# Optimization experiments

Measured on AMD Instinct MI355X. Metric: run time of the kernel, lower is better.

## Reference

```python
import jax, jax.numpy as jnp
import numpy as np

B, T, C, NH = 8, 1024, 768, 12

def setup_inputs() -> dict:
    key = jax.random.key(0)
    k1, k2, k3 = jax.random.split(key, 3)
    x = jax.random.normal(k1, (B, T, C), dtype=jnp.float32)
    Wqkv = jax.random.normal(k2, (C, 3 * C), dtype=jnp.float32) * 0.02
    bqkv = jnp.zeros((3 * C,), dtype=jnp.float32)
    Wproj = jax.random.normal(k3, (C, C), dtype=jnp.float32) * 0.02
    bproj = jnp.zeros((C,), dtype=jnp.float32)
    return {"x": x, "Wqkv": Wqkv, "bqkv": bqkv, "Wproj": Wproj, "bproj": bproj}

def reference(x, Wqkv, bqkv, Wproj, bproj):
    b, t, c = x.shape
    hs = c // NH
    qkv = x @ Wqkv + bqkv  # [B,T,3C]
    q, k, v = jnp.split(qkv, 3, axis=2)
    # [B,T,C] -> [B,NH,T,hs]
    q = q.reshape(b, t, NH, hs).transpose(0, 2, 1, 3)
    k = k.reshape(b, t, NH, hs).transpose(0, 2, 1, 3)
    v = v.reshape(b, t, NH, hs).transpose(0, 2, 1, 3)
    att = jnp.einsum('bhqd,bhkd->bhqk', q, k) * (hs ** -0.5)
    causal = jnp.tril(jnp.ones((t, t), dtype=bool))
    att = jnp.where(causal[None, None], att, jnp.finfo(att.dtype).min)
    att = jax.nn.softmax(att, axis=-1)
    y = jnp.einsum('bhqk,bhkd->bhqd', att, v)
    y = y.transpose(0, 2, 1, 3).reshape(b, t, c)
    return y @ Wproj + bproj
```

## Files before the change

### kernel.cpp

```cpp
#include <hip/hip_runtime.h>

constexpr int Bb  = 8;
constexpr int Tt  = 1024;
constexpr int Cc  = 768;
constexpr int NHh = 12;
constexpr int HS  = 64;
constexpr int C3  = 3 * Cc;

typedef short bf16x8 __attribute__((ext_vector_type(8)));
typedef float f32x4  __attribute__((ext_vector_type(4)));

__device__ inline short bf16r(float f) {
    unsigned u = __float_as_uint(f);
    u += 0x7FFF + ((u >> 16) & 1);
    return (short)(u >> 16);
}
__device__ inline short bf16h(float f) {
    return (short)((__float_as_uint(f) + 0x8000u) >> 16);
}

__global__ __launch_bounds__(256)
void prep_all(const float* __restrict__ x, const float* __restrict__ Wqkv,
              const float* __restrict__ Wproj, short* __restrict__ xb,
              short* __restrict__ wqkvT, short* __restrict__ wprojT) {
    int bid = blockIdx.x;
    constexpr int XBLK = (Bb * Tt * Cc) / 1024;
    constexpr int QT   = (C3 / 32) * (Cc / 32);
    if (bid < XBLK) {
        const int i = (bid * 256 + threadIdx.x) * 4;
        float4 v = *(const float4*)(x + i);
        short4 o;
        o.x = bf16r(v.x); o.y = bf16r(v.y); o.z = bf16r(v.z); o.w = bf16r(v.w);
        *(short4*)(xb + i) = o;
        return;
    }
    bid -= XBLK;
    const float* src; short* dst; int C;
    if (bid < QT) { src = Wqkv;  dst = wqkvT;  C = C3; }
    else          { bid -= QT; src = Wproj; dst = wprojT; C = Cc; }
    const int tcx = bid % (C / 32), tcy = bid / (C / 32);
    __shared__ short tile[32][33];
    const int tx = threadIdx.x & 31, ty = threadIdx.x >> 5;
#pragma unroll
    for (int rr = 0; rr < 4; ++rr) {
        const int r = ty * 4 + rr;
        tile[r][tx] = bf16r(src[(size_t)(tcy * 32 + r) * C + tcx * 32 + tx]);
    }
    __syncthreads();
#pragma unroll
    for (int rr = 0; rr < 4; ++rr) {
        const int orow = ty * 4 + rr;
        dst[(size_t)(tcx * 32 + orow) * Cc + tcy * 32 + tx] = tile[tx][orow];
    }
}

__global__ __launch_bounds__(256)
void transpose_v(const short* __restrict__ qkv, short* __restrict__ vt) {
    __shared__ short tile[64][65];
    const int bh = blockIdx.y;
    const int b = bh / NHh, h = bh % NHh;
    const int t0 = blockIdx.x * 64;
    const int tx = threadIdx.x & 63, ty = threadIdx.x >> 6;
    const short* src = qkv + ((size_t)b * Tt + t0) * C3 + 2 * Cc + h * HS;
#pragma unroll
    for (int r = 0; r < 16; ++r)
        tile[ty * 16 + r][tx] = src[(size_t)(ty * 16 + r) * C3 + tx];
    __syncthreads();
    short* dst = vt + (size_t)bh * HS * Tt + t0;
#pragma unroll
    for (int r = 0; r < 16; ++r)
        dst[(size_t)(ty * 16 + r) * Tt + tx] = tile[tx][ty * 16 + r];
}

template <int MI, int OB>
__global__ __launch_bounds__(256)
void gemm_mfma_bias(const short* __restrict__ A, const short* __restrict__ Bt,
                    const float* __restrict__ bias, void* __restrict__ Cout,
                    int M, int N, int K) {
    constexpr int TM = MI * 32;
    __shared__ __align__(16) short Als[2][TM * 32];
    __shared__ __align__(16) short Bls[2][128 * 32];

    const int t = threadIdx.x, w = t >> 6, lane = t & 63;

    const int flat = blockIdx.y * gridDim.x + blockIdx.x;
    const int mPer = gridDim.y >> 3;
    const int idx  = flat >> 3;
    const int my   = (flat & 7) * mPer + idx % mPer;
    const int nx   = idx / mPer;
    const int m0 = my * TM, n0 = nx * 128;

    const int sr = t >> 2;
    const int lg = ((t & 3) ^ ((t >> 3) & 3)) * 8;

    const short* Ag[MI / 2];
#pragma unroll
    for (int q = 0; q < MI / 2; ++q)
        Ag[q] = A + (size_t)(m0 + q * 64 + sr) * K + lg;
    const short* Bg[2];
#pragma unroll
    for (int q = 0; q < 2; ++q)
        Bg[q] = Bt + (size_t)(n0 + q * 64 + sr) * K + lg;

    const int wq = w * 1024;

    const int wm = (w >> 1) * (MI * 16), wn = (w & 1) * 64;
    const int laneM = lane & 15, laneG = lane >> 4;
    const int kx = (laneG ^ ((laneM >> 1) & 3)) * 8;

    f32x4 acc[MI][4] = {};

    const int nk = K / 32;

#pragma unroll
    for (int q = 0; q < MI / 2; ++q)
        __builtin_amdgcn_global_load_lds(
            (const __attribute__((address_space(1))) void*)(Ag[q]),
            (__attribute__((address_space(3))) void*)((char*)&Als[0][0] + q * 4096 + wq), 16, 0, 0);
#pragma unroll
    for (int q = 0; q < 2; ++q)
        __builtin_amdgcn_global_load_lds(
            (const __attribute__((address_space(1))) void*)(Bg[q]),
            (__attribute__((address_space(3))) void*)((char*)&Bls[0][0] + q * 4096 + wq), 16, 0, 0);

    for (int kt = 0; kt < nk; ++kt) {
        __syncthreads();

        const short* Ab = &Als[kt & 1][0];
        const short* Bb = &Bls[kt & 1][0];
        bf16x8 af[MI], bfr[4];
#pragma unroll
        for (int i = 0; i < MI; ++i)
            af[i] = *(const bf16x8*)&Ab[(wm + i * 16 + laneM) * 32 + kx];
#pragma unroll
        for (int j = 0; j < 4; ++j)
            bfr[j] = *(const bf16x8*)&Bb[(wn + j * 16 + laneM) * 32 + kx];

        if (kt + 1 < nk) {
            const int b = (kt + 1) & 1, ko = (kt + 1) * 32;
#pragma unroll
            for (int q = 0; q < MI / 2; ++q)
                __builtin_amdgcn_global_load_lds(
                    (const __attribute__((address_space(1))) void*)(Ag[q] + ko),
                    (__attribute__((address_space(3))) void*)((char*)&Als[b][0] + q * 4096 + wq), 16, 0, 0);
#pragma unroll
            for (int q = 0; q < 2; ++q)
                __builtin_amdgcn_global_load_lds(
                    (const __attribute__((address_space(1))) void*)(Bg[q] + ko),
                    (__attribute__((address_space(3))) void*)((char*)&Bls[b][0] + q * 4096 + wq), 16, 0, 0);
        }

#pragma unroll
        for (int i = 0; i < MI; ++i)
#pragma unroll
            for (int j = 0; j < 4; ++j)
                acc[i][j] = __builtin_amdgcn_mfma_f32_16x16x32_bf16(
                    af[i], bfr[j], acc[i][j], 0, 0, 0);
    }

    const int rowBase = m0 + wm + laneG * 4;
    const int colBase = n0 + wn + laneM;
#pragma unroll
    for (int j = 0; j < 4; ++j) {
        const int col = colBase + j * 16;
        const float bv = bias[col];
#pragma unroll
        for (int i = 0; i < MI; ++i) {
#pragma unroll
            for (int r = 0; r < 4; ++r) {
                const int row = rowBase + i * 16 + r;
                const float v = acc[i][j][r] + bv;
                if (OB) ((short*)Cout)[(size_t)row * N + col] = bf16r(v);
                else    ((float*)Cout)[(size_t)row * N + col] = v;
            }
        }
    }
}

__global__ __launch_bounds__(256)
void flash_attn(const short* __restrict__ qkv, const short* __restrict__ vt,
                short* __restrict__ y) {
    const int bh = blockIdx.x % (Bb * NHh);
    const int pi = blockIdx.x / (Bb * NHh);
    const int h  = bh % NHh, b = bh / NHh;
    const int t = threadIdx.x, w = t >> 6, lane = t & 63;
    const int laneM = lane & 15, laneG = lane >> 4;

    __shared__ short Kls[2][64 * 64];
    __shared__ short Vls[2][64 * 64];
    __shared__ short Pls[4][16 * 72];

    const size_t bT = (size_t)b * Tt;

    bf16x8 onesb;
#pragma unroll
    for (int j = 0; j < 8; ++j) onesb[j] = (short)0x3F80;

    const int srow = t >> 3;
    const int gpos = t & 7;
    const int gs0 = (gpos ^ (srow & 7)) * 8;

    const short* Kbase = qkv + (bT + srow) * C3 + Cc + h * HS + gs0;
    const short* Vbase = vt + ((size_t)bh * HS + srow) * Tt + gs0;

    auto stage = [&](int kt, int buf) {
        const short* Kg = Kbase + (size_t)kt * 64 * C3;
        const short* Vg = Vbase + kt * 64;
        char* KB = (char*)&Kls[buf][0] + w * 1024;
        char* VB = (char*)&Vls[buf][0] + w * 1024;
        __builtin_amdgcn_global_load_lds(
            (const __attribute__((address_space(1))) void*)Kg,
            (__attribute__((address_space(3))) void*)(KB), 16, 0, 0);
        __builtin_amdgcn_global_load_lds(
            (const __attribute__((address_space(1))) void*)(Kg + 32 * C3),
            (__attribute__((address_space(3))) void*)(KB + 4096), 16, 0, 0);
        __builtin_amdgcn_global_load_lds(
            (const __attribute__((address_space(1))) void*)Vg,
            (__attribute__((address_space(3))) void*)(VB), 16, 0, 0);
        __builtin_amdgcn_global_load_lds(
            (const __attribute__((address_space(1))) void*)(Vg + 32 * Tt),
            (__attribute__((address_space(3))) void*)(VB + 4096), 16, 0, 0);
    };

    constexpr float cexp = 0.18033688f;
    constexpr float moff = -5.7707801f;

#pragma unroll 1
    for (int sub = 0; sub < 2; ++sub) {
        const int qt = sub ? (15 - pi) : pi;
        const int q0 = qt * 64;

        const short* qp = qkv + (bT + q0 + w * 16 + laneM) * C3 + h * HS;
        const bf16x8 qf0 = *(const bf16x8*)(qp + laneG * 8);
        const bf16x8 qf1 = *(const bf16x8*)(qp + 32 + laneG * 8);

        f32x4 oacc[4] = {};
        f32x4 lacc   = {};

        __syncthreads();
        stage(0, 0);

#pragma unroll 1
        for (int kt = 0; kt <= qt; ++kt) {
            __syncthreads();
            if (kt < qt) stage(kt + 1, (kt + 1) & 1);

            const short* Kb = &Kls[kt & 1][0];
            const short* Vb = &Vls[kt & 1][0];

            f32x4 sacc[4] = {};
            __builtin_amdgcn_s_setprio(1);
#pragma unroll
            for (int ks = 0; ks < 2; ++ks) {
                const bf16x8 qf = ks ? qf1 : qf0;
#pragma unroll
                for (int nb = 0; nb < 4; ++nb) {
                    const int key = nb * 16 + laneM;
                    const bf16x8 kf = *(const bf16x8*)
                        &Kb[key * 64 + (((ks << 2) + laneG) ^ (key & 7)) * 8];
                    sacc[nb] = __builtin_amdgcn_mfma_f32_16x16x32_bf16(
                        qf, kf, sacc[nb], 0, 0, 0);
                }
            }
            __builtin_amdgcn_s_setprio(0);

            if (kt == qt) {
#pragma unroll
                for (int nb = 0; nb < 4; ++nb) {
                    const int col = nb * 16 + laneM;
#pragma unroll
                    for (int r = 0; r < 4; ++r) {
                        const int row = w * 16 + laneG * 4 + r;
                        if (col > row) sacc[nb][r] = -1e30f;
                    }
                }
            }

            short* Pw = &Pls[w][0];
#pragma unroll
            for (int r = 0; r < 4; ++r)
#pragma unroll
                for (int nb = 0; nb < 4; ++nb) {
                    const float pv = exp2f(fmaf(sacc[nb][r], cexp, moff));
                    Pw[(laneG * 4 + r) * 72 + nb * 16 + laneM] = bf16h(pv);
                }

            __builtin_amdgcn_s_setprio(1);
#pragma unroll
            for (int ks = 0; ks < 2; ++ks) {
                const bf16x8 pf = *(const bf16x8*)&Pw[laneM * 72 + ks * 32 + laneG * 8];
                lacc = __builtin_amdgcn_mfma_f32_16x16x32_bf16(pf, onesb, lacc, 0, 0, 0);
#pragma unroll
                for (int nb = 0; nb < 4; ++nb) {
                    const int d = nb * 16 + laneM;
                    const bf16x8 vf = *(const bf16x8*)
                        &Vb[d * 64 + (((ks << 2) + laneG) ^ (d & 7)) * 8];
                    oacc[nb] = __builtin_amdgcn_mfma_f32_16x16x32_bf16(
                        pf, vf, oacc[nb], 0, 0, 0);
                }
            }
            __builtin_amdgcn_s_setprio(0);
        }

        short* yp = y + (bT + q0 + w * 16) * Cc + h * HS;
#pragma unroll
        for (int r = 0; r < 4; ++r) {
            const float inv = 1.f / lacc[r];
#pragma unroll
            for (int nb = 0; nb < 4; ++nb)
                yp[(size_t)(laneG * 4 + r) * Cc + nb * 16 + laneM] = bf16r(oacc[nb][r] * inv);
        }
    }
}

extern "C" void kernel_launch(void* const* d_in, const int* in_sizes, int n_in,
                              void* d_out, int out_size, void* d_ws, size_t ws_size,
                              hipStream_t stream) {
    const float* x     = (const float*)d_in[0];
    const float* Wqkv  = (const float*)d_in[1];
    const float* bqkv  = (const float*)d_in[2];
    const float* Wproj = (const float*)d_in[3];
    const float* bproj = (const float*)d_in[4];

    constexpr int M = Bb * Tt;
    short* xb     = (short*)d_ws;
    short* wqkvT  = xb     + (size_t)M * Cc;
    short* wprojT = wqkvT  + (size_t)C3 * Cc;
    short* qkv    = wprojT + (size_t)Cc * Cc;
    short* yatt   = qkv    + (size_t)M * C3;
    short* vt     = yatt   + (size_t)M * Cc;

    constexpr int PREP_BLOCKS = (M * Cc) / 1024 + (C3 / 32) * (Cc / 32) + (Cc / 32) * (Cc / 32);
    prep_all<<<dim3(PREP_BLOCKS), dim3(256), 0, stream>>>(x, Wqkv, Wproj, xb, wqkvT, wprojT);

    gemm_mfma_bias<4, 1><<<dim3(C3 / 128, M / 128), dim3(256), 0, stream>>>(
        xb, wqkvT, bqkv, qkv, M, C3, Cc);

    transpose_v<<<dim3(Tt / 64, Bb * NHh), dim3(256), 0, stream>>>(qkv, vt);

    flash_attn<<<dim3(Bb * NHh * 8), dim3(256), 0, stream>>>(qkv, vt, yatt);

    gemm_mfma_bias<2, 0><<<dim3(Cc / 128, M / 64), dim3(256), 0, stream>>>(
        yatt, wprojT, bproj, (float*)d_out, M, Cc, Cc);
}
```

Baseline: 182.7 us.

## Pass softmax probabilities via cross-lane permutes instead of LDS round-trip

The QK^T MFMA operands are swapped so each lane holds scores transposed (keys along rows), letting probabilities be packed to bf16 with v_cvt_pk_bf16_f32 and redistributed into the PV A-operand layout via ds_bpermute rather than being written to and re-read from a per-wave LDS buffer. The causal mask indexing is adjusted for the transposed layout, the P shared buffer is removed, and launch bounds request 5 waves/blocks per SIMD. This removes LDS stores/loads and the associated waits per tile, at the cost of 16 bpermutes plus selects per tile and possible register pressure from the occupancy hint.

```diff
diff --git a/kernel.cpp b/kernel.cpp
--- a/kernel.cpp
+++ b/kernel.cpp
@@ -9,14 +9,12 @@
 
 typedef short bf16x8 __attribute__((ext_vector_type(8)));
 typedef float f32x4  __attribute__((ext_vector_type(4)));
+typedef int   i32x4  __attribute__((ext_vector_type(4)));
 
 __device__ inline short bf16r(float f) {
     unsigned u = __float_as_uint(f);
     u += 0x7FFF + ((u >> 16) & 1);
     return (short)(u >> 16);
-}
-__device__ inline short bf16h(float f) {
-    return (short)((__float_as_uint(f) + 0x8000u) >> 16);
 }
 
 __global__ __launch_bounds__(256)
@@ -177,7 +175,7 @@
     }
 }
 
-__global__ __launch_bounds__(256)
+__global__ __launch_bounds__(256, 5)
 void flash_attn(const short* __restrict__ qkv, const short* __restrict__ vt,
                 short* __restrict__ y) {
     const int bh = blockIdx.x % (Bb * NHh);
@@ -188,7 +186,6 @@
 
     __shared__ short Kls[2][64 * 64];
     __shared__ short Vls[2][64 * 64];
-    __shared__ short Pls[4][16 * 72];
 
     const size_t bT = (size_t)b * Tt;
 
@@ -202,6 +199,10 @@
 
     const short* Kbase = qkv + (bT + srow) * C3 + Cc + h * HS + gs0;
     const short* Vbase = vt + ((size_t)bh * HS + srow) * Tt + gs0;
+
+    const int addrLo = (laneM + ((laneG & 1) << 5)) << 2;
+    const int addrHi = addrLo + 64;
+    const bool hi32 = (lane >= 32);
 
     auto stage = [&](int kt, int buf) {
         const short* Kg = Kbase + (size_t)kt * 64 * C3;
@@ -259,7 +260,7 @@
                     const bf16x8 kf = *(const bf16x8*)
                         &Kb[key * 64 + (((ks << 2) + laneG) ^ (key & 7)) * 8];
                     sacc[nb] = __builtin_amdgcn_mfma_f32_16x16x32_bf16(
-                        qf, kf, sacc[nb], 0, 0, 0);
+                        kf, qf, sacc[nb], 0, 0, 0);
                 }
             }
             __builtin_amdgcn_s_setprio(0);
@@ -267,36 +268,51 @@
             if (kt == qt) {
 #pragma unroll
                 for (int nb = 0; nb < 4; ++nb) {
-                    const int col = nb * 16 + laneM;
+                    const int qrow = w * 16 + laneM;
 #pragma unroll
                     for (int r = 0; r < 4; ++r) {
-                        const int row = w * 16 + laneG * 4 + r;
-                        if (col > row) sacc[nb][r] = -1e30f;
+                        const int key = nb * 16 + laneG * 4 + r;
+                        if (key > qrow) sacc[nb][r] = -1e30f;
                     }
                 }
             }
 
-            short* Pw = &Pls[w][0];
-#pragma unroll
-            for (int r = 0; r < 4; ++r)
-#pragma unroll
-                for (int nb = 0; nb < 4; ++nb) {
-                    const float pv = exp2f(fmaf(sacc[nb][r], cexp, moff));
-                    Pw[(laneG * 4 + r) * 72 + nb * 16 + laneM] = bf16h(pv);
+            unsigned pk[4][2];
+#pragma unroll
+            for (int nb = 0; nb < 4; ++nb) {
+                const float e0 = exp2f(fmaf(sacc[nb][0], cexp, moff));
+                const float e1 = exp2f(fmaf(sacc[nb][1], cexp, moff));
+                const float e2 = exp2f(fmaf(sacc[nb][2], cexp, moff));
+                const float e3 = exp2f(fmaf(sacc[nb][3], cexp, moff));
+                asm("v_cvt_pk_bf16_f32 %0, %1, %2" : "=v"(pk[nb][0]) : "v"(e0), "v"(e1));
+                asm("v_cvt_pk_bf16_f32 %0, %1, %2" : "=v"(pk[nb][1]) : "v"(e2), "v"(e3));
+            }
+
+            bf16x8 pf[2];
+#pragma unroll
+            for (int ks = 0; ks < 2; ++ks) {
+                i32x4 dw;
+#pragma unroll
+                for (int jd = 0; jd < 4; ++jd) {
+                    const int addr = (jd & 2) ? addrHi : addrLo;
+                    const int lo = __builtin_amdgcn_ds_bpermute(addr, (int)pk[2 * ks][jd & 1]);
+                    const int hi = __builtin_amdgcn_ds_bpermute(addr, (int)pk[2 * ks + 1][jd & 1]);
+                    dw[jd] = hi32 ? hi : lo;
                 }
+                pf[ks] = *(const bf16x8*)&dw;
+            }
 
             __builtin_amdgcn_s_setprio(1);
 #pragma unroll
             for (int ks = 0; ks < 2; ++ks) {
-                const bf16x8 pf = *(const bf16x8*)&Pw[laneM * 72 + ks * 32 + laneG * 8];
-                lacc = __builtin_amdgcn_mfma_f32_16x16x32_bf16(pf, onesb, lacc, 0, 0, 0);
+                lacc = __builtin_amdgcn_mfma_f32_16x16x32_bf16(pf[ks], onesb, lacc, 0, 0, 0);
 #pragma unroll
                 for (int nb = 0; nb < 4; ++nb) {
                     const int d = nb * 16 + laneM;
                     const bf16x8 vf = *(const bf16x8*)
                         &Vb[d * 64 + (((ks << 2) + laneG) ^ (d & 7)) * 8];
                     oacc[nb] = __builtin_amdgcn_mfma_f32_16x16x32_bf16(
-                        pf, vf, oacc[nb], 0, 0, 0);
+                        pf[ks], vf, oacc[nb], 0, 0, 0);
                 }
             }
             __builtin_amdgcn_s_setprio(0);
```

Result: no change. 183.8 us (+0.6%).

## Use two waves per flash-attention block with 32 query rows each

Applied to the files above, without the earlier changes.

The attention kernel drops from four waves of 16 query rows to two waves of 32 rows each. K and V fragments are read from LDS once into registers and reused across both 16-row groups, which halves LDS fragment traffic per MFMA. Each thread now issues four staging loads per tile instead of two. The cost is higher register pressure per wave, and there are half as many waves per block to hide latency, which may reduce occupancy or overlap.

```diff
diff --git a/kernel.cpp b/kernel.cpp
--- a/kernel.cpp
+++ b/kernel.cpp
@@ -177,7 +177,7 @@
     }
 }
 
-__global__ __launch_bounds__(256)
+__global__ __launch_bounds__(128)
 void flash_attn(const short* __restrict__ qkv, const short* __restrict__ vt,
                 short* __restrict__ y) {
     const int bh = blockIdx.x % (Bb * NHh);
@@ -188,7 +188,7 @@
 
     __shared__ short Kls[2][64 * 64];
     __shared__ short Vls[2][64 * 64];
-    __shared__ short Pls[4][16 * 72];
+    __shared__ short Pls[2][32 * 72];
 
     const size_t bT = (size_t)b * Tt;
 
@@ -208,18 +208,16 @@
         const short* Vg = Vbase + kt * 64;
         char* KB = (char*)&Kls[buf][0] + w * 1024;
         char* VB = (char*)&Vls[buf][0] + w * 1024;
-        __builtin_amdgcn_global_load_lds(
-            (const __attribute__((address_space(1))) void*)Kg,
-            (__attribute__((address_space(3))) void*)(KB), 16, 0, 0);
-        __builtin_amdgcn_global_load_lds(
-            (const __attribute__((address_space(1))) void*)(Kg + 32 * C3),
-            (__attribute__((address_space(3))) void*)(KB + 4096), 16, 0, 0);
-        __builtin_amdgcn_global_load_lds(
-            (const __attribute__((address_space(1))) void*)Vg,
-            (__attribute__((address_space(3))) void*)(VB), 16, 0, 0);
-        __builtin_amdgcn_global_load_lds(
-            (const __attribute__((address_space(1))) void*)(Vg + 32 * Tt),
-            (__attribute__((address_space(3))) void*)(VB + 4096), 16, 0, 0);
+#pragma unroll
+        for (int i = 0; i < 4; ++i)
+            __builtin_amdgcn_global_load_lds(
+                (const __attribute__((address_space(1))) void*)(Kg + (size_t)i * 16 * C3),
+                (__attribute__((address_space(3))) void*)(KB + i * 2048), 16, 0, 0);
+#pragma unroll
+        for (int i = 0; i < 4; ++i)
+            __builtin_amdgcn_global_load_lds(
+                (const __attribute__((address_space(1))) void*)(Vg + (size_t)i * 16 * Tt),
+                (__attribute__((address_space(3))) void*)(VB + i * 2048), 16, 0, 0);
     };
 
     constexpr float cexp = 0.18033688f;
@@ -230,12 +228,16 @@
         const int qt = sub ? (15 - pi) : pi;
         const int q0 = qt * 64;
 
-        const short* qp = qkv + (bT + q0 + w * 16 + laneM) * C3 + h * HS;
-        const bf16x8 qf0 = *(const bf16x8*)(qp + laneG * 8);
-        const bf16x8 qf1 = *(const bf16x8*)(qp + 32 + laneG * 8);
-
-        f32x4 oacc[4] = {};
-        f32x4 lacc   = {};
+        const short* qp0 = qkv + (bT + q0 + w * 32 + laneM) * C3 + h * HS;
+        const short* qp1 = qp0 + (size_t)16 * C3;
+        bf16x8 qf[2][2];
+        qf[0][0] = *(const bf16x8*)(qp0 + laneG * 8);
+        qf[0][1] = *(const bf16x8*)(qp0 + 32 + laneG * 8);
+        qf[1][0] = *(const bf16x8*)(qp1 + laneG * 8);
+        qf[1][1] = *(const bf16x8*)(qp1 + 32 + laneG * 8);
+
+        f32x4 oacc[2][4] = {};
+        f32x4 lacc[2]    = {};
 
         __syncthreads();
         stage(0, 0);
@@ -248,67 +250,91 @@
             const short* Kb = &Kls[kt & 1][0];
             const short* Vb = &Vls[kt & 1][0];
 
-            f32x4 sacc[4] = {};
-            __builtin_amdgcn_s_setprio(1);
-#pragma unroll
-            for (int ks = 0; ks < 2; ++ks) {
-                const bf16x8 qf = ks ? qf1 : qf0;
+            bf16x8 kf[2][4];
+#pragma unroll
+            for (int ks = 0; ks < 2; ++ks)
 #pragma unroll
                 for (int nb = 0; nb < 4; ++nb) {
                     const int key = nb * 16 + laneM;
-                    const bf16x8 kf = *(const bf16x8*)
+                    kf[ks][nb] = *(const bf16x8*)
                         &Kb[key * 64 + (((ks << 2) + laneG) ^ (key & 7)) * 8];
-                    sacc[nb] = __builtin_amdgcn_mfma_f32_16x16x32_bf16(
-                        qf, kf, sacc[nb], 0, 0, 0);
                 }
+
+            f32x4 sacc[2][4] = {};
+            __builtin_amdgcn_s_setprio(1);
+#pragma unroll
+            for (int mg = 0; mg < 2; ++mg)
+#pragma unroll
+                for (int ks = 0; ks < 2; ++ks)
+#pragma unroll
+                    for (int nb = 0; nb < 4; ++nb)
+                        sacc[mg][nb] = __builtin_amdgcn_mfma_f32_16x16x32_bf16(
+                            qf[mg][ks], kf[ks][nb], sacc[mg][nb], 0, 0, 0);
+            __builtin_amdgcn_s_setprio(0);
+
+            if (kt == qt) {
+#pragma unroll
+                for (int mg = 0; mg < 2; ++mg)
+#pragma unroll
+                    for (int nb = 0; nb < 4; ++nb) {
+                        const int col = nb * 16 + laneM;
+#pragma unroll
+                        for (int r = 0; r < 4; ++r) {
+                            const int row = w * 32 + mg * 16 + laneG * 4 + r;
+                            if (col > row) sacc[mg][nb][r] = -1e30f;
+                        }
+                    }
             }
-            __builtin_amdgcn_s_setprio(0);
-
-            if (kt == qt) {
-#pragma unroll
-                for (int nb = 0; nb < 4; ++nb) {
-                    const int col = nb * 16 + laneM;
-#pragma unroll
-                    for (int r = 0; r < 4; ++r) {
-                        const int row = w * 16 + laneG * 4 + r;
-                        if (col > row) sacc[nb][r] = -1e30f;
+
+            short* Pw = &Pls[w][0];
+#pragma unroll
+            for (int mg = 0; mg < 2; ++mg)
+#pragma unroll
+                for (int r = 0; r < 4; ++r)
+#pragma unroll
+                    for (int nb = 0; nb < 4; ++nb) {
+                        const float pv = exp2f(fmaf(sacc[mg][nb][r], cexp, moff));
+                        Pw[(mg * 16 + laneG * 4 + r) * 72 + nb * 16 + laneM] = bf16h(pv);
                     }
-                }
-            }
-
-            short* Pw = &Pls[w][0];
-#pragma unroll
-            for (int r = 0; r < 4; ++r)
-#pragma unroll
-                for (int nb = 0; nb < 4; ++nb) {
-                    const float pv = exp2f(fmaf(sacc[nb][r], cexp, moff));
-                    Pw[(laneG * 4 + r) * 72 + nb * 16 + laneM] = bf16h(pv);
-                }
-
-            __builtin_amdgcn_s_setprio(1);
-#pragma unroll
-            for (int ks = 0; ks < 2; ++ks) {
-                const bf16x8 pf = *(const bf16x8*)&Pw[laneM * 72 + ks * 32 + laneG * 8];
-                lacc = __builtin_amdgcn_mfma_f32_16x16x32_bf16(pf, onesb, lacc, 0, 0, 0);
+
+            bf16x8 vf[2][4];
+#pragma unroll
+            for (int ks = 0; ks < 2; ++ks)
 #pragma unroll
                 for (int nb = 0; nb < 4; ++nb) {
                     const int d = nb * 16 + laneM;
-                    const bf16x8 vf = *(const bf16x8*)
+                    vf[ks][nb] = *(const bf16x8*)
                         &Vb[d * 64 + (((ks << 2) + laneG) ^ (d & 7)) * 8];
-                    oacc[nb] = __builtin_amdgcn_mfma_f32_16x16x32_bf16(
-                        pf, vf, oacc[nb], 0, 0, 0);
                 }
-            }
+
+            __builtin_amdgcn_s_setprio(1);
+#pragma unroll
+            for (int mg = 0; mg < 2; ++mg)
+#pragma unroll
+                for (int ks = 0; ks < 2; ++ks) {
+                    const bf16x8 pf = *(const bf16x8*)
+                        &Pw[(mg * 16 + laneM) * 72 + ks * 32 + laneG * 8];
+                    lacc[mg] = __builtin_amdgcn_mfma_f32_16x16x32_bf16(
+                        pf, onesb, lacc[mg], 0, 0, 0);
+#pragma unroll
+                    for (int nb = 0; nb < 4; ++nb)
+                        oacc[mg][nb] = __builtin_amdgcn_mfma_f32_16x16x32_bf16(
+                            pf, vf[ks][nb], oacc[mg][nb], 0, 0, 0);
+                }
             __builtin_amdgcn_s_setprio(0);
         }
 
-        short* yp = y + (bT + q0 + w * 16) * Cc + h * HS;
-#pragma unroll
-        for (int r = 0; r < 4; ++r) {
-            const float inv = 1.f / lacc[r];
-#pragma unroll
-            for (int nb = 0; nb < 4; ++nb)
-                yp[(size_t)(laneG * 4 + r) * Cc + nb * 16 + laneM] = bf16r(oacc[nb][r] * inv);
+#pragma unroll
+        for (int mg = 0; mg < 2; ++mg) {
+            short* yp = y + (bT + q0 + w * 32 + mg * 16) * Cc + h * HS;
+#pragma unroll
+            for (int r = 0; r < 4; ++r) {
+                const float inv = 1.f / lacc[mg][r];
+#pragma unroll
+                for (int nb = 0; nb < 4; ++nb)
+                    yp[(size_t)(laneG * 4 + r) * Cc + nb * 16 + laneM] =
+                        bf16r(oacc[mg][nb][r] * inv);
+            }
         }
     }
 }
@@ -338,7 +364,7 @@
 
     transpose_v<<<dim3(Tt / 64, Bb * NHh), dim3(256), 0, stream>>>(qkv, vt);
 
-    flash_attn<<<dim3(Bb * NHh * 8), dim3(256), 0, stream>>>(qkv, vt, yatt);
+    flash_attn<<<dim3(Bb * NHh * 8), dim3(128), 0, stream>>>(qkv, vt, yatt);
 
     gemm_mfma_bias<2, 0><<<dim3(Cc / 128, M / 64), dim3(256), 0, stream>>>(
         yatt, wprojT, bproj, (float*)d_out, M, Cc, Cc);
```

New measurement: 191.9 us. 5.0% more time.
